# Kernel tuning notes

Hardware: AMD Instinct MI355X
Metric: run time of the kernel (lower is better)

Reference implementation:

```python
import jax, jax.numpy as jnp
import numpy as np

B, S, D = 2, 4096, 768
H, HD = 12, 64  # num_head, head_dim


def setup_inputs() -> dict:
    key = jax.random.key(0)
    ks = jax.random.split(key, 10)
    s = 0.02
    return {
        "X": jax.random.normal(ks[0], (B, S, D), dtype=jnp.float32),
        "mask": jnp.ones((B, S), dtype=jnp.float32),
        "Wq": jax.random.normal(ks[1], (D, H * HD), dtype=jnp.float32) * s,
        "bq": jnp.zeros((H * HD,), dtype=jnp.float32),
        "Wk": jax.random.normal(ks[2], (D, H * HD), dtype=jnp.float32) * s,
        "bk": jnp.zeros((H * HD,), dtype=jnp.float32),
        "Wv": jax.random.normal(ks[3], (D, H * HD), dtype=jnp.float32) * s,
        "bv": jnp.zeros((H * HD,), dtype=jnp.float32),
        "Wo": jax.random.normal(ks[4], (H * HD, D), dtype=jnp.float32) * s,
        "bo": jnp.zeros((D,), dtype=jnp.float32),
    }


def _split_heads(x):
    # [B,S,H*HD] -> [B,H,S,HD]
    return x.reshape(B, S, H, HD).transpose(0, 2, 1, 3)


def reference(X, mask, Wq, bq, Wk, bk, Wv, bv, Wo, bo):
    Q = _split_heads(X @ Wq + bq)
    K = _split_heads(X @ Wk + bk)
    V = _split_heads(X @ Wv + bv)
    # scores: [B,H,S,S]
    dot = jnp.einsum("bhqd,bhkd->bhqk", Q, K) / np.sqrt(HD).astype(np.float32)
    dot = dot - 1e6 * (1.0 - mask[:, None, None, :])
    attn = jax.nn.softmax(dot, axis=-1)
    ctx = jnp.einsum("bhqk,bhkd->bhqd", attn, V)
    # combine heads: [B,H,S,HD] -> [B,S,H*HD]
    ctx = ctx.transpose(0, 2, 1, 3).reshape(B, S, H * HD)
    return ctx @ Wo + bo
```

## Files before the change

### kernel.cpp

```cpp
#include <hip/hip_runtime.h>

#define BATCH   2
#define S_LEN   4096
#define D_MODEL 768
#define NH      12
#define HDIM    64
#define MROWS   (BATCH * S_LEN)
#define QBLK    128
#define KVBLK   64
#define NT      (S_LEN / KVBLK)
#define NXB     (MROWS * D_MODEL / 4 / 256)
#define NTW     2304
#define LOG2E   1.4426950408889634f

typedef float f32x4  __attribute__((ext_vector_type(4)));
typedef float f32x16 __attribute__((ext_vector_type(16)));
typedef short bf16x8 __attribute__((ext_vector_type(8)));

#if __has_builtin(__builtin_amdgcn_exp2f)
#define EXP2(x) __builtin_amdgcn_exp2f(x)
#else
#define EXP2(x) exp2f(x)
#endif

static __device__ __forceinline__ unsigned short f2bf(float f) {
  union { float f; unsigned u; } v; v.f = f;
  unsigned r = v.u + 0x7fffu + ((v.u >> 16) & 1u);
  return (unsigned short)(r >> 16);
}

static __device__ __forceinline__ unsigned cvtpk(float lo, float hi) {
  unsigned r;
  asm("v_cvt_pk_bf16_f32 %0, %1, %2" : "=v"(r) : "v"(lo), "v"(hi));
  return r;
}

typedef __attribute__((address_space(1))) const unsigned int as1_cuint;
typedef __attribute__((address_space(3))) unsigned int as3_uint;
static __device__ __forceinline__ void gload_lds16(const unsigned short* g,
                                                   unsigned short* l) {
  __builtin_amdgcn_global_load_lds((as1_cuint*)g, (as3_uint*)l, 16, 0, 0);
}

template <int BASE>
static __device__ __forceinline__ bf16x8 pack_frag(const f32x16& s) {
  unsigned a0 = cvtpk(s[BASE + 0], s[BASE + 1]);
  unsigned b0 = cvtpk(s[BASE + 4], s[BASE + 5]);
  asm("v_permlane32_swap_b32 %0, %1" : "+v"(a0), "+v"(b0));
  unsigned a1 = cvtpk(s[BASE + 2], s[BASE + 3]);
  unsigned b1 = cvtpk(s[BASE + 6], s[BASE + 7]);
  asm("v_permlane32_swap_b32 %0, %1" : "+v"(a1), "+v"(b1));
  union { unsigned w[4]; bf16x8 v; } u;
  u.w[0] = a0; u.w[1] = a1; u.w[2] = b0; u.w[3] = b1;
  return u.v;
}

#define Z16 {0.f,0.f,0.f,0.f,0.f,0.f,0.f,0.f,0.f,0.f,0.f,0.f,0.f,0.f,0.f,0.f}

__global__ __launch_bounds__(256) void prepass(
    const float* __restrict__ X, unsigned short* __restrict__ Xb,
    const float* __restrict__ mask, float* __restrict__ madd, int* __restrict__ flag,
    const float* __restrict__ W0, const float* __restrict__ W1,
    const float* __restrict__ W2, const float* __restrict__ W3,
    unsigned short* __restrict__ T0, unsigned short* __restrict__ T1,
    unsigned short* __restrict__ T2, unsigned short* __restrict__ T3) {
  __shared__ float tile[32][33];
  __shared__ int ok[4];
  int bid = blockIdx.x;
  int t = threadIdx.x;
  if (bid < NXB) {
    int i = bid * 256 + t;
    float4 v = ((const float4*)X)[i];
    ushort4 o;
    o.x = f2bf(v.x); o.y = f2bf(v.y); o.z = f2bf(v.z); o.w = f2bf(v.w);
    ((ushort4*)Xb)[i] = o;
    return;
  }
  if (bid == NXB) {
    int all1 = 1;
    #pragma unroll
    for (int i = 0; i < MROWS / 256; ++i) {
      int idx = i * 256 + t;
      float m = mask[idx];
      madd[idx] = (-1e6f * LOG2E) * (1.0f - m);
      all1 &= (m == 1.0f);
    }
    all1 = __all(all1) ? 1 : 0;
    if ((t & 63) == 0) ok[t >> 6] = all1;
    __syncthreads();
    if (t == 0) *flag = ok[0] & ok[1] & ok[2] & ok[3];
    return;
  }
  int w2 = bid - (NXB + 1);
  int zz = w2 / 576;
  int r = w2 - zz * 576;
  int bxi = r % 24, byi = r / 24;
  const float* W; unsigned short* T;
  if (zz == 0) { W = W0; T = T0; }
  else if (zz == 1) { W = W1; T = T1; }
  else if (zz == 2) { W = W2; T = T2; }
  else { W = W3; T = T3; }
  int tx = t & 31, ty = t >> 5;
  int bx = bxi * 32, by = byi * 32;
  #pragma unroll
  for (int i = ty; i < 32; i += 8) tile[i][tx] = W[(size_t)(by + i) * D_MODEL + bx + tx];
  __syncthreads();
  #pragma unroll
  for (int i = ty; i < 32; i += 8)
    T[(size_t)(bx + i) * D_MODEL + by + tx] = f2bf(tile[tx][i]);
}

__global__ __launch_bounds__(256) void qkv_gemm(
    const unsigned short* __restrict__ Xb,
    const unsigned short* __restrict__ Wqt, const unsigned short* __restrict__ Wkt,
    const unsigned short* __restrict__ Wvt,
    const float* __restrict__ bq, const float* __restrict__ bk, const float* __restrict__ bv,
    unsigned short* __restrict__ Qo, unsigned short* __restrict__ Ko,
    unsigned short* __restrict__ Vto) {
  __shared__ unsigned short As[128 * 64];
  __shared__ unsigned short Bs[128 * 64];
  int zz = blockIdx.z;
  const unsigned short* Wt = zz == 0 ? Wqt : (zz == 1 ? Wkt : Wvt);
  const float* bias = zz == 0 ? bq : (zz == 1 ? bk : bv);
  int tid = threadIdx.x;
  int w = tid >> 6, lane = tid & 63, lr = lane & 15, lg = lane >> 4;
  int wr = w >> 1, wc = w & 1;
  int mb = blockIdx.x * 128, nb = blockIdx.y * 128;
  const unsigned short* Ag = Xb + (size_t)(mb + (tid >> 3)) * D_MODEL + (tid & 7) * 8;
  const unsigned short* Bg = Wt + (size_t)(nb + (tid >> 3)) * D_MODEL + (tid & 7) * 8;
  unsigned short* Al = As + (size_t)tid * 8;
  unsigned short* Bl = Bs + (size_t)tid * 8;
  f32x4 acc[4][4];
  #pragma unroll
  for (int m = 0; m < 4; ++m)
    #pragma unroll
    for (int n = 0; n < 4; ++n) acc[m][n] = (f32x4){0.f, 0.f, 0.f, 0.f};
  for (int kb = 0; kb < D_MODEL / 64; ++kb) {
    __syncthreads();
    #pragma unroll
    for (int i = 0; i < 4; ++i) {
      gload_lds16(Ag + (size_t)(i * 32) * D_MODEL + kb * 64, Al + i * 2048);
      gload_lds16(Bg + (size_t)(i * 32) * D_MODEL + kb * 64, Bl + i * 2048);
    }
    __syncthreads();
    #pragma unroll
    for (int kk = 0; kk < 2; ++kk) {
      bf16x8 af[4], bfv[4];
      #pragma unroll
      for (int m = 0; m < 4; ++m)
        af[m] = *(const bf16x8*)(As + (wr * 64 + m * 16 + lr) * 64 + kk * 32 + lg * 8);
      #pragma unroll
      for (int n = 0; n < 4; ++n)
        bfv[n] = *(const bf16x8*)(Bs + (wc * 64 + n * 16 + lr) * 64 + kk * 32 + lg * 8);
      #pragma unroll
      for (int m = 0; m < 4; ++m)
        #pragma unroll
        for (int n = 0; n < 4; ++n)
          acc[m][n] = __builtin_amdgcn_mfma_f32_16x16x32_bf16(af[m], bfv[n], acc[m][n], 0, 0, 0);
    }
  }
  #pragma unroll
  for (int n = 0; n < 4; ++n) {
    int nc = nb + wc * 64 + n * 16 + lr;
    float bia = bias[nc];
    int h = nc >> 6, hd = nc & 63;
    #pragma unroll
    for (int m = 0; m < 4; ++m) {
      #pragma unroll
      for (int r = 0; r < 4; ++r) {
        int mr = mb + wr * 64 + m * 16 + lg * 4 + r;
        int b = mr >> 12, s = mr & 4095;
        float val = acc[m][n][r] + bia;
        if (zz == 0)
          Qo[((size_t)(b * NH + h) * S_LEN + s) * HDIM + hd] = f2bf(val * 0.125f * LOG2E);
        else if (zz == 1)
          Ko[((size_t)(b * NH + h) * S_LEN + s) * HDIM + hd] = f2bf(val);
        else
          Vto[((size_t)(b * NH + h) * HDIM + hd) * S_LEN + s] = f2bf(val);
      }
    }
  }
}

__global__ __launch_bounds__(256) void attn_kernel(
    const unsigned short* __restrict__ Q, const unsigned short* __restrict__ K,
    const unsigned short* __restrict__ Vt, const float* __restrict__ madd,
    const int* __restrict__ allones_p, unsigned short* __restrict__ Ctx) {
  __shared__ unsigned short Ks[2][64][72];
  __shared__ unsigned short Vs[2][64][72];
  int lin = blockIdx.x;
  int wg = (lin & 7) * 96 + (lin >> 3);
  int qb = wg & 31, bh = wg >> 5;
  int b = bh / NH, h = bh % NH;
  int tid = threadIdx.x;
  int w = tid >> 6, lane = tid & 63;
  int lq = lane & 31, hi = lane >> 5;
  const unsigned short* Qb = Q + (size_t)bh * S_LEN * HDIM;
  const unsigned short* Kb = K + (size_t)bh * S_LEN * HDIM;
  const unsigned short* Vb = Vt + (size_t)bh * HDIM * S_LEN;
  const float* maddb = madd + (size_t)b * S_LEN;
  const int allones = *allones_p;

  int qrow = qb * QBLK + w * 32 + lq;
  bf16x8 qf0 = *(const bf16x8*)(Qb + (size_t)qrow * HDIM + 0 * 16 + hi * 8);
  bf16x8 qf1 = *(const bf16x8*)(Qb + (size_t)qrow * HDIM + 1 * 16 + hi * 8);
  bf16x8 qf2 = *(const bf16x8*)(Qb + (size_t)qrow * HDIM + 2 * 16 + hi * 8);
  bf16x8 qf3 = *(const bf16x8*)(Qb + (size_t)qrow * HDIM + 3 * 16 + hi * 8);

  f32x16 acc0 = Z16, acc1 = Z16;
  float l_run = 0.f;

  int srow = tid >> 3, sseg = (tid & 7) * 8;
  uint4 ka, kc, va, vc;

  ka = *(const uint4*)(Kb + (size_t)srow * HDIM + sseg);
  kc = *(const uint4*)(Kb + (size_t)(srow + 32) * HDIM + sseg);
  va = *(const uint4*)(Vb + (size_t)srow * S_LEN + sseg);
  vc = *(const uint4*)(Vb + (size_t)(srow + 32) * S_LEN + sseg);
  *(uint4*)&Ks[0][srow][sseg]      = ka;
  *(uint4*)&Ks[0][srow + 32][sseg] = kc;
  *(uint4*)&Vs[0][srow][sseg]      = va;
  *(uint4*)&Vs[0][srow + 32][sseg] = vc;
  __syncthreads();

  for (int t = 0; t < NT; ++t) {
    int cur = t & 1;
    int kbase = t * KVBLK;
    if (t + 1 < NT) {
      int nb2 = kbase + KVBLK;
      ka = *(const uint4*)(Kb + (size_t)(nb2 + srow) * HDIM + sseg);
      kc = *(const uint4*)(Kb + (size_t)(nb2 + srow + 32) * HDIM + sseg);
      va = *(const uint4*)(Vb + (size_t)srow * S_LEN + nb2 + sseg);
      vc = *(const uint4*)(Vb + (size_t)(srow + 32) * S_LEN + nb2 + sseg);
    }
    f32x16 s0 = Z16, s1 = Z16;
    #pragma unroll
    for (int c = 0; c < 4; ++c) {
      bf16x8 kf0 = *(const bf16x8*)(&Ks[cur][lq][c * 16 + hi * 8]);
      bf16x8 kf1 = *(const bf16x8*)(&Ks[cur][32 + lq][c * 16 + hi * 8]);
      bf16x8 qf = c == 0 ? qf0 : (c == 1 ? qf1 : (c == 2 ? qf2 : qf3));
      s0 = __builtin_amdgcn_mfma_f32_32x32x16_bf16(kf0, qf, s0, 0, 0, 0);
      s1 = __builtin_amdgcn_mfma_f32_32x32x16_bf16(kf1, qf, s1, 0, 0, 0);
    }
    if (!allones) {
      #pragma unroll
      for (int g = 0; g < 4; ++g) {
        float4 m0 = *(const float4*)(maddb + kbase + g * 8 + hi * 4);
        float4 m1 = *(const float4*)(maddb + kbase + 32 + g * 8 + hi * 4);
        s0[g * 4 + 0] += m0.x; s0[g * 4 + 1] += m0.y;
        s0[g * 4 + 2] += m0.z; s0[g * 4 + 3] += m0.w;
        s1[g * 4 + 0] += m1.x; s1[g * 4 + 1] += m1.y;
        s1[g * 4 + 2] += m1.z; s1[g * 4 + 3] += m1.w;
      }
    }
    float psA = 0.f, psB = 0.f, psC = 0.f, psD = 0.f;
    #pragma unroll
    for (int r = 0; r < 4; ++r) {
      s0[r]      = EXP2(s0[r]);      psA += s0[r];
      s0[r + 4]  = EXP2(s0[r + 4]);  psB += s0[r + 4];
      s0[r + 8]  = EXP2(s0[r + 8]);  psC += s0[r + 8];
      s0[r + 12] = EXP2(s0[r + 12]); psD += s0[r + 12];
    }
    #pragma unroll
    for (int r = 0; r < 4; ++r) {
      s1[r]      = EXP2(s1[r]);      psA += s1[r];
      s1[r + 4]  = EXP2(s1[r + 4]);  psB += s1[r + 4];
      s1[r + 8]  = EXP2(s1[r + 8]);  psC += s1[r + 8];
      s1[r + 12] = EXP2(s1[r + 12]); psD += s1[r + 12];
    }
    float psum = (psA + psB) + (psC + psD);
    psum += __shfl_xor(psum, 32, 64);
    l_run += psum;
    bf16x8 pa0 = pack_frag<0>(s0);
    bf16x8 pa1 = pack_frag<8>(s0);
    bf16x8 pa2 = pack_frag<0>(s1);
    bf16x8 pa3 = pack_frag<8>(s1);
    #pragma unroll
    for (int c = 0; c < 4; ++c) {
      bf16x8 pa = c == 0 ? pa0 : (c == 1 ? pa1 : (c == 2 ? pa2 : pa3));
      bf16x8 vf0 = *(const bf16x8*)(&Vs[cur][lq][c * 16 + hi * 8]);
      bf16x8 vf1 = *(const bf16x8*)(&Vs[cur][32 + lq][c * 16 + hi * 8]);
      acc0 = __builtin_amdgcn_mfma_f32_32x32x16_bf16(pa, vf0, acc0, 0, 0, 0);
      acc1 = __builtin_amdgcn_mfma_f32_32x32x16_bf16(pa, vf1, acc1, 0, 0, 0);
    }
    if (t + 1 < NT) {
      int nxt = cur ^ 1;
      *(uint4*)&Ks[nxt][srow][sseg]      = ka;
      *(uint4*)&Ks[nxt][srow + 32][sseg] = kc;
      *(uint4*)&Vs[nxt][srow][sseg]      = va;
      *(uint4*)&Vs[nxt][srow + 32][sseg] = vc;
      __syncthreads();
    }
  }
  #pragma unroll
  for (int r = 0; r < 16; ++r) {
    int qr = (r & 3) + 8 * (r >> 2) + 4 * hi;
    float lv = __shfl(l_run, qr, 64);
    float rl = 1.0f / lv;
    int qglob = qb * QBLK + w * 32 + qr;
    size_t base = ((size_t)(b * S_LEN + qglob)) * D_MODEL + h * HDIM;
    Ctx[base + lq]      = f2bf(acc0[r] * rl);
    Ctx[base + 32 + lq] = f2bf(acc1[r] * rl);
  }
}

__global__ __launch_bounds__(256) void out_gemm(
    const unsigned short* __restrict__ Ctx, const unsigned short* __restrict__ Wot,
    const float* __restrict__ bo, float* __restrict__ Out) {
  __shared__ unsigned short As[128 * 64];
  __shared__ unsigned short Bs[128 * 64];
  int tid = threadIdx.x;
  int w = tid >> 6, lane = tid & 63, lr = lane & 15, lg = lane >> 4;
  int wr = w >> 1, wc = w & 1;
  int mb = blockIdx.x * 128, nb = blockIdx.y * 128;
  const unsigned short* Ag = Ctx + (size_t)(mb + (tid >> 3)) * D_MODEL + (tid & 7) * 8;
  const unsigned short* Bg = Wot + (size_t)(nb + (tid >> 3)) * D_MODEL + (tid & 7) * 8;
  unsigned short* Al = As + (size_t)tid * 8;
  unsigned short* Bl = Bs + (size_t)tid * 8;
  f32x4 acc[4][4];
  #pragma unroll
  for (int m = 0; m < 4; ++m)
    #pragma unroll
    for (int n = 0; n < 4; ++n) acc[m][n] = (f32x4){0.f, 0.f, 0.f, 0.f};
  for (int kb = 0; kb < D_MODEL / 64; ++kb) {
    __syncthreads();
    #pragma unroll
    for (int i = 0; i < 4; ++i) {
      gload_lds16(Ag + (size_t)(i * 32) * D_MODEL + kb * 64, Al + i * 2048);
      gload_lds16(Bg + (size_t)(i * 32) * D_MODEL + kb * 64, Bl + i * 2048);
    }
    __syncthreads();
    #pragma unroll
    for (int kk = 0; kk < 2; ++kk) {
      bf16x8 af[4], bfv[4];
      #pragma unroll
      for (int m = 0; m < 4; ++m)
        af[m] = *(const bf16x8*)(As + (wr * 64 + m * 16 + lr) * 64 + kk * 32 + lg * 8);
      #pragma unroll
      for (int n = 0; n < 4; ++n)
        bfv[n] = *(const bf16x8*)(Bs + (wc * 64 + n * 16 + lr) * 64 + kk * 32 + lg * 8);
      #pragma unroll
      for (int m = 0; m < 4; ++m)
        #pragma unroll
        for (int n = 0; n < 4; ++n)
          acc[m][n] = __builtin_amdgcn_mfma_f32_16x16x32_bf16(af[m], bfv[n], acc[m][n], 0, 0, 0);
    }
  }
  #pragma unroll
  for (int n = 0; n < 4; ++n) {
    int nc = nb + wc * 64 + n * 16 + lr;
    float bia = bo[nc];
    #pragma unroll
    for (int m = 0; m < 4; ++m) {
      #pragma unroll
      for (int r = 0; r < 4; ++r) {
        int mr = mb + wr * 64 + m * 16 + lg * 4 + r;
        Out[(size_t)mr * D_MODEL + nc] = acc[m][n][r] + bia;
      }
    }
  }
}


extern "C" void kernel_launch(void* const* d_in, const int* in_sizes, int n_in,
                              void* d_out, int out_size, void* d_ws, size_t ws_size,
                              hipStream_t stream) {
  const float* X    = (const float*)d_in[0];
  const float* mask = (const float*)d_in[1];
  const float* Wq   = (const float*)d_in[2];
  const float* bq   = (const float*)d_in[3];
  const float* Wk   = (const float*)d_in[4];
  const float* bk   = (const float*)d_in[5];
  const float* Wv   = (const float*)d_in[6];
  const float* bv   = (const float*)d_in[7];
  const float* Wo   = (const float*)d_in[8];
  const float* bo   = (const float*)d_in[9];
  float* out = (float*)d_out;
  char* ws = (char*)d_ws;

  const size_t XB_OFF   = 0;
  const size_t WQT_OFF  = 12582912;
  const size_t WKT_OFF  = WQT_OFF + 1179648;
  const size_t WVT_OFF  = WKT_OFF + 1179648;
  const size_t WOT_OFF  = WVT_OFF + 1179648;
  const size_t Q_OFF    = WOT_OFF + 1179648;
  const size_t K_OFF    = Q_OFF + 12582912;
  const size_t VT_OFF   = K_OFF + 12582912;
  const size_t CTX_OFF  = VT_OFF + 12582912;
  const size_t MADD_OFF = CTX_OFF + 12582912;
  const size_t FLAG_OFF = MADD_OFF + MROWS * 4;

  unsigned short* Xb  = (unsigned short*)(ws + XB_OFF);
  unsigned short* Wqt = (unsigned short*)(ws + WQT_OFF);
  unsigned short* Wkt = (unsigned short*)(ws + WKT_OFF);
  unsigned short* Wvt = (unsigned short*)(ws + WVT_OFF);
  unsigned short* Wot = (unsigned short*)(ws + WOT_OFF);
  unsigned short* Qw  = (unsigned short*)(ws + Q_OFF);
  unsigned short* Kw  = (unsigned short*)(ws + K_OFF);
  unsigned short* Vtw = (unsigned short*)(ws + VT_OFF);
  unsigned short* Ctx = (unsigned short*)(ws + CTX_OFF);
  float* madd = (float*)(ws + MADD_OFF);
  int* flag   = (int*)(ws + FLAG_OFF);

  prepass<<<dim3(NXB + 1 + NTW), 256, 0, stream>>>(
      X, Xb, mask, madd, flag, Wq, Wk, Wv, Wo, Wqt, Wkt, Wvt, Wot);
  qkv_gemm<<<dim3(MROWS / 128, D_MODEL / 128, 3), 256, 0, stream>>>(
      Xb, Wqt, Wkt, Wvt, bq, bk, bv, Qw, Kw, Vtw);
  attn_kernel<<<dim3((S_LEN / QBLK) * (BATCH * NH)), 256, 0, stream>>>(
      Qw, Kw, Vtw, madd, flag, Ctx);
  out_gemm<<<dim3(MROWS / 128, D_MODEL / 128), 256, 0, stream>>>(Ctx, Wot, bo, out);
}
```

Baseline: 253.8 us.

## Load K/V tiles directly global-to-LDS with XOR-swizzled layout in attention

Replaces the register-staged K/V prefetch (global load to registers, then store to LDS after compute) with direct global-to-LDS 16-byte loads via a gload_lds16 helper. The padded LDS rows are replaced by an XOR swizzle on 8-element groups, applied on both the load and the MFMA fragment reads, to avoid bank conflicts. This frees VGPRs and removes the LDS store instructions. It relies on the helper (defined elsewhere) and on async load completion being covered by the existing barrier, which may need explicit vmcnt waits.

```diff
diff --git a/kernel.cpp b/kernel.cpp
--- a/kernel.cpp
+++ b/kernel.cpp
@@ -186,8 +186,8 @@
     const unsigned short* __restrict__ Q, const unsigned short* __restrict__ K,
     const unsigned short* __restrict__ Vt, const float* __restrict__ madd,
     const int* __restrict__ allones_p, unsigned short* __restrict__ Ctx) {
-  __shared__ unsigned short Ks[2][64][72];
-  __shared__ unsigned short Vs[2][64][72];
+  __shared__ unsigned short Ks[2][64][64];
+  __shared__ unsigned short Vs[2][64][64];
   int lin = blockIdx.x;
   int wg = (lin & 7) * 96 + (lin >> 3);
   int qb = wg & 31, bh = wg >> 5;
@@ -210,34 +210,43 @@
   f32x16 acc0 = Z16, acc1 = Z16;
   float l_run = 0.f;
 
-  int srow = tid >> 3, sseg = (tid & 7) * 8;
-  uint4 ka, kc, va, vc;
-
-  ka = *(const uint4*)(Kb + (size_t)srow * HDIM + sseg);
-  kc = *(const uint4*)(Kb + (size_t)(srow + 32) * HDIM + sseg);
-  va = *(const uint4*)(Vb + (size_t)srow * S_LEN + sseg);
-  vc = *(const uint4*)(Vb + (size_t)(srow + 32) * S_LEN + sseg);
-  *(uint4*)&Ks[0][srow][sseg]      = ka;
-  *(uint4*)&Ks[0][srow + 32][sseg] = kc;
-  *(uint4*)&Vs[0][srow][sseg]      = va;
-  *(uint4*)&Vs[0][srow + 32][sseg] = vc;
+  int r0 = tid >> 3;
+  int g0 = (tid & 7) ^ (r0 & 7);
+  int r1 = (tid + 256) >> 3;
+  int g1 = (tid & 7) ^ (r1 & 7);
+  const unsigned short* kg0 = Kb + (size_t)r0 * HDIM + g0 * 8;
+  const unsigned short* kg1 = Kb + (size_t)r1 * HDIM + g1 * 8;
+  const unsigned short* vg0 = Vb + (size_t)r0 * S_LEN + g0 * 8;
+  const unsigned short* vg1 = Vb + (size_t)r1 * S_LEN + g1 * 8;
+
+  {
+    unsigned short* kd = &Ks[0][0][0] + tid * 8;
+    unsigned short* vd = &Vs[0][0][0] + tid * 8;
+    gload_lds16(kg0, kd);
+    gload_lds16(kg1, kd + 2048);
+    gload_lds16(vg0, vd);
+    gload_lds16(vg1, vd + 2048);
+  }
   __syncthreads();
 
   for (int t = 0; t < NT; ++t) {
     int cur = t & 1;
     int kbase = t * KVBLK;
     if (t + 1 < NT) {
-      int nb2 = kbase + KVBLK;
-      ka = *(const uint4*)(Kb + (size_t)(nb2 + srow) * HDIM + sseg);
-      kc = *(const uint4*)(Kb + (size_t)(nb2 + srow + 32) * HDIM + sseg);
-      va = *(const uint4*)(Vb + (size_t)srow * S_LEN + nb2 + sseg);
-      vc = *(const uint4*)(Vb + (size_t)(srow + 32) * S_LEN + nb2 + sseg);
+      int off = kbase + KVBLK;
+      unsigned short* kd = &Ks[cur ^ 1][0][0] + tid * 8;
+      unsigned short* vd = &Vs[cur ^ 1][0][0] + tid * 8;
+      gload_lds16(kg0 + (size_t)off * HDIM, kd);
+      gload_lds16(kg1 + (size_t)off * HDIM, kd + 2048);
+      gload_lds16(vg0 + off, vd);
+      gload_lds16(vg1 + off, vd + 2048);
     }
     f32x16 s0 = Z16, s1 = Z16;
     #pragma unroll
     for (int c = 0; c < 4; ++c) {
-      bf16x8 kf0 = *(const bf16x8*)(&Ks[cur][lq][c * 16 + hi * 8]);
-      bf16x8 kf1 = *(const bf16x8*)(&Ks[cur][32 + lq][c * 16 + hi * 8]);
+      int gq = (((c << 1) | hi) ^ (lq & 7)) * 8;
+      bf16x8 kf0 = *(const bf16x8*)(&Ks[cur][lq][gq]);
+      bf16x8 kf1 = *(const bf16x8*)(&Ks[cur][32 + lq][gq]);
       bf16x8 qf = c == 0 ? qf0 : (c == 1 ? qf1 : (c == 2 ? qf2 : qf3));
       s0 = __builtin_amdgcn_mfma_f32_32x32x16_bf16(kf0, qf, s0, 0, 0, 0);
       s1 = __builtin_amdgcn_mfma_f32_32x32x16_bf16(kf1, qf, s1, 0, 0, 0);
@@ -277,20 +286,14 @@
     bf16x8 pa3 = pack_frag<8>(s1);
     #pragma unroll
     for (int c = 0; c < 4; ++c) {
+      int gq = (((c << 1) | hi) ^ (lq & 7)) * 8;
       bf16x8 pa = c == 0 ? pa0 : (c == 1 ? pa1 : (c == 2 ? pa2 : pa3));
-      bf16x8 vf0 = *(const bf16x8*)(&Vs[cur][lq][c * 16 + hi * 8]);
-      bf16x8 vf1 = *(const bf16x8*)(&Vs[cur][32 + lq][c * 16 + hi * 8]);
+      bf16x8 vf0 = *(const bf16x8*)(&Vs[cur][lq][gq]);
+      bf16x8 vf1 = *(const bf16x8*)(&Vs[cur][32 + lq][gq]);
       acc0 = __builtin_amdgcn_mfma_f32_32x32x16_bf16(pa, vf0, acc0, 0, 0, 0);
       acc1 = __builtin_amdgcn_mfma_f32_32x32x16_bf16(pa, vf1, acc1, 0, 0, 0);
     }
-    if (t + 1 < NT) {
-      int nxt = cur ^ 1;
-      *(uint4*)&Ks[nxt][srow][sseg]      = ka;
-      *(uint4*)&Ks[nxt][srow + 32][sseg] = kc;
-      *(uint4*)&Vs[nxt][srow][sseg]      = va;
-      *(uint4*)&Vs[nxt][srow + 32][sseg] = vc;
-      __syncthreads();
-    }
+    if (t + 1 < NT) __syncthreads();
   }
   #pragma unroll
   for (int r = 0; r < 16; ++r) {
```

After: 272.7 us. 1.07x slower.
